# Kernel optimization log

Hardware: AMD Instinct MI355X
Metric: run time of the kernel (lower is better)

The kernel has to match this reference:

```python
import jax, jax.numpy as jnp
import numpy as np

B, S, D, F, E, K = 64, 512, 512, 2048, 8, 2


def setup_inputs() -> dict:
    key = jax.random.key(0)
    k0, k1, k2, k3 = jax.random.split(key, 4)
    x = jax.random.normal(k0, (B, S, D), dtype=jnp.float32)
    Wr = jax.random.normal(k1, (D, E), dtype=jnp.float32) * (D ** -0.5)
    br = jnp.zeros((E,), dtype=jnp.float32)
    W1 = jax.random.normal(k2, (E, D, F), dtype=jnp.float32) * (D ** -0.5)
    b1 = jnp.zeros((E, F), dtype=jnp.float32)
    W2 = jax.random.normal(k3, (E, F, D), dtype=jnp.float32) * (F ** -0.5)
    b2 = jnp.zeros((E, D), dtype=jnp.float32)
    return {"x": x, "Wr": Wr, "br": br, "W1": W1, "b1": b1, "W2": W2, "b2": b2}


def reference(x, Wr, br, W1, b1, W2, b2):
    orig_shape = x.shape
    t = x.reshape(-1, orig_shape[-1])          # [T, D] flattened tokens
    logits = t @ Wr + br                       # [T, E] router logits
    gates = jax.nn.softmax(logits, axis=-1)
    top_vals, top_idx = jax.lax.top_k(gates, K)      # [T, K]
    top_vals = top_vals / top_vals.sum(axis=-1, keepdims=True)
    # combine weight per (token, expert); zero unless expert is in token's top-k
    onehot = jax.nn.one_hot(top_idx, E, dtype=t.dtype)      # [T, K, E]
    combine = jnp.einsum('tk,tke->te', top_vals, onehot)    # [T, E]
    out = jnp.zeros_like(t)
    for e in range(E):  # small fixed expert count
        h = jax.nn.relu(t @ W1[e] + b1[e])     # [T, F]
        y = h @ W2[e] + b2[e]                  # [T, D]
        out = out + combine[:, e:e + 1] * y
    return out.reshape(orig_shape)
```

## Files before the change

kernel.cpp:

```cpp
#include <hip/hip_runtime.h>

#define T_TOKENS 32768
#define DIM 512
#define FDIM 2048
#define NEXP 8

typedef __attribute__((ext_vector_type(4))) float f32x4;
typedef __attribute__((ext_vector_type(8))) short bf16x8;

__device__ __forceinline__ unsigned short f2bf(float f) {
  unsigned int u = __float_as_uint(f);
  u += 0x7FFFu + ((u >> 16) & 1u);
  return (unsigned short)(u >> 16);
}

#define LGKM_BARRIER()                                        \
  do {                                                        \
    asm volatile("s_waitcnt lgkmcnt(0)" ::: "memory");        \
    __builtin_amdgcn_s_barrier();                             \
  } while (0)

__global__ void pack_w1_kernel(const float* __restrict__ W1, unsigned short* __restrict__ W1p) {
  __shared__ float L[512][17];
  const int b = blockIdx.x;
  const int e = b >> 7, ft = b & 127;
  const int t = threadIdx.x;
  const int c = t & 15, r0 = t >> 4;
  const float* src = W1 + (long)e * 512 * 2048 + ft * 16 + c;
  #pragma unroll
  for (int ch = 0; ch < 32; ch++) {
    int r = ch * 16 + r0;
    L[r][c] = src[(long)r * 2048];
  }
  __syncthreads();
  #pragma unroll
  for (int s = 0; s < 4; s++) {
    int slot = s * 256 + t;
    int kci = slot >> 6, l = slot & 63;
    unsigned short tmp[8];
    #pragma unroll
    for (int j = 0; j < 8; j++)
      tmp[j] = f2bf(L[kci * 32 + (l >> 4) * 8 + j][l & 15]);
    *(ushort4*)(W1p + ((long)b * 16 + kci) * 512 + l * 8)     = *(ushort4*)&tmp[0];
    *(ushort4*)(W1p + ((long)b * 16 + kci) * 512 + l * 8 + 4) = *(ushort4*)&tmp[4];
  }
}

__global__ void pack_w2_kernel(const float* __restrict__ W2, unsigned short* __restrict__ W2p) {
  __shared__ float L[512][17];
  const int b = blockIdx.x;
  const int e = b >> 5, dt = b & 31;
  const int t = threadIdx.x;
  const int c = t & 15, r0 = t >> 4;
  for (int ch = 0; ch < 4; ch++) {
    if (ch) __syncthreads();
    const float* src = W2 + ((long)e * 2048 + ch * 512) * 512 + dt * 16 + c;
    #pragma unroll
    for (int cc = 0; cc < 32; cc++) {
      int r = cc * 16 + r0;
      L[r][c] = src[(long)r * 512];
    }
    __syncthreads();
    #pragma unroll
    for (int s = 0; s < 4; s++) {
      int slot = s * 256 + t;
      int kciL = slot >> 6, l = slot & 63;
      unsigned short tmp[8];
      #pragma unroll
      for (int j = 0; j < 8; j++)
        tmp[j] = f2bf(L[kciL * 32 + (l >> 4) * 8 + j][l & 15]);
      long tt = (long)(e * 64 + ch * 16 + kciL) * 32 + dt;
      *(ushort4*)(W2p + tt * 512 + l * 8)     = *(ushort4*)&tmp[0];
      *(ushort4*)(W2p + tt * 512 + l * 8 + 4) = *(ushort4*)&tmp[4];
    }
  }
}

__global__ void router_kernel(const float* __restrict__ x, const float* __restrict__ Wr,
                              const float* __restrict__ br, int* __restrict__ counts,
                              int* __restrict__ tok_list, float* __restrict__ wt_list,
                              int* __restrict__ slots) {
  __shared__ float WrS[NEXP][DIM];
  __shared__ int lcnt[NEXP];
  __shared__ int lbase[NEXP];
  const int tid = threadIdx.x;
  for (int i = tid; i < NEXP * DIM; i += 256) {
    int e = i >> 9, d = i & (DIM - 1);
    WrS[e][d] = Wr[d * NEXP + e];
  }
  if (tid < NEXP) lcnt[tid] = 0;
  __syncthreads();

  const int t = blockIdx.x * 256 + tid;
  const float* xr = x + (long)t * DIM;
  float acc[NEXP];
  #pragma unroll
  for (int e = 0; e < NEXP; e++) acc[e] = br[e];
  for (int d = 0; d < DIM; d += 4) {
    const float4 xv = *(const float4*)(xr + d);
    #pragma unroll
    for (int e = 0; e < NEXP; e++)
      acc[e] += xv.x * WrS[e][d] + xv.y * WrS[e][d + 1] +
                xv.z * WrS[e][d + 2] + xv.w * WrS[e][d + 3];
  }
  int e0 = 0; float v0 = acc[0];
  #pragma unroll
  for (int e = 1; e < NEXP; e++) if (acc[e] > v0) { v0 = acc[e]; e0 = e; }
  int e1 = -1; float v1 = -3.4e38f;
  #pragma unroll
  for (int e = 0; e < NEXP; e++) if (e != e0 && acc[e] > v1) { v1 = acc[e]; e1 = e; }
  float w0 = 1.f / (1.f + __expf(v1 - v0));
  float w1 = 1.f - w0;

  int l0 = atomicAdd(&lcnt[e0], 1);
  int l1 = atomicAdd(&lcnt[e1], 1);
  __syncthreads();
  if (tid < NEXP) lbase[tid] = atomicAdd(&counts[tid], lcnt[tid]);
  __syncthreads();
  int s0 = lbase[e0] + l0;
  tok_list[e0 * T_TOKENS + s0] = t; wt_list[e0 * T_TOKENS + s0] = w0;
  int s1 = lbase[e1] + l1;
  tok_list[e1 * T_TOKENS + s1] = t; wt_list[e1 * T_TOKENS + s1] = w1;
  if (slots) {
    slots[2 * t]     = e0 * T_TOKENS + s0;
    slots[2 * t + 1] = e1 * T_TOKENS + s1;
  }
}

#define LD8(dst, ptr, kbase)                                    \
  _Pragma("unroll")                                             \
  for (int i = 0; i < 8; i++)                                   \
    dst[i] = *(const bf16x8*)((ptr) + (kbase + i) * 512);

#define MF8(src, kbase)                                                            \
  _Pragma("unroll")                                                                \
  for (int i = 0; i < 8; i++) {                                                    \
    int kci = (kbase) + i;                                                         \
    int xo = ((kci * 4 + g) ^ xsw) << 3;                                           \
    _Pragma("unroll")                                                              \
    for (int mt = 0; mt < 4; mt++) {                                               \
      bf16x8 af = *(const bf16x8*)&Xs[(mt * 16 + ln) * 512 + xo];                  \
      H[mt] = __builtin_amdgcn_mfma_f32_16x16x32_bf16(af, src[i], H[mt], 0, 0, 0); \
    }                                                                              \
  }

#define LD_W2(klbase)                                                             \
  _Pragma("unroll")                                                               \
  for (int kl = klbase; kl < klbase + 2; kl++) {                                  \
    const unsigned short* w2b =                                                   \
        W2p + ((long)((e * 64 + (fc >> 5) + kl) * 32 + wave * 4) * 64 + lane) * 8;\
    _Pragma("unroll")                                                             \
    for (int nt = 0; nt < 4; nt++)                                                \
      w2r[kl][nt] = *(const bf16x8*)(w2b + nt * 512);                             \
  }

template <bool USE_PARTIAL>
__global__ __launch_bounds__(512, 2) void ffn_kernel(
    const float* __restrict__ x,
    const unsigned short* __restrict__ W1p,
    const unsigned short* __restrict__ W2p,
    const float* __restrict__ b1, const float* __restrict__ b2,
    const int* __restrict__ counts,
    const int* __restrict__ tok_list, const float* __restrict__ wt_list,
    float* __restrict__ partial,
    float* __restrict__ out) {
  __shared__ unsigned short Xs[64 * 512];
  __shared__ unsigned short Hs[64 * 128];

  const int e = blockIdx.x & 7;
  const int tile = blockIdx.x >> 3;
  const int cnt = counts[e];
  const int m0 = tile * 64;
  if (m0 >= cnt) return;
  const int rows = min(64, cnt - m0);

  int pbase = 0;
  if (USE_PARTIAL) {
    #pragma unroll
    for (int i = 0; i < NEXP; i++) pbase += (i < e) ? counts[i] : 0;
  }

  const int tid = threadIdx.x;
  const int wave = tid >> 6, lane = tid & 63;
  const int g = lane >> 4, ln = lane & 15;

  #pragma unroll 4
  for (int c = tid; c < 64 * 128; c += 512) {
    int r = c >> 7, q = c & 127;
    ushort4 bv = {0, 0, 0, 0};
    if (r < rows) {
      int tk = tok_list[e * T_TOKENS + m0 + r];
      const f32x4 v = __builtin_nontemporal_load((const f32x4*)(x + (long)tk * DIM + q * 4));
      bv.x = f2bf(v[0]); bv.y = f2bf(v[1]); bv.z = f2bf(v[2]); bv.w = f2bf(v[3]);
    }
    int addr = r * 512 + ((((q >> 1) ^ (r & 7)) << 3) | ((q & 1) << 2));
    *(ushort4*)&Xs[addr] = bv;
  }
  LGKM_BARRIER();

  const f32x4 zero4 = {0.f, 0.f, 0.f, 0.f};
  f32x4 Yacc[4][4];
  #pragma unroll
  for (int a = 0; a < 4; a++)
    #pragma unroll
    for (int b = 0; b < 4; b++) Yacc[a][b] = zero4;

  const int xsw = ln & 7;

  const unsigned short* const w1b_first =
      W1p + ((long)(e * 128 + wave) * 16) * 512 + lane * 8;
  const unsigned short* w1b = w1b_first;

  bf16x8 wA[8], wB[8], w2r[4][4];
  LD8(wA, w1b, 0);

  for (int fc = 0; fc < FDIM; fc += 128) {
    unsigned short* Hp = &Hs[0];
    f32x4 H[4];
    #pragma unroll
    for (int mt = 0; mt < 4; mt++) H[mt] = zero4;

    LD8(wB, w1b, 8);
    __builtin_amdgcn_s_setprio(1);
    MF8(wA, 0);
    __builtin_amdgcn_s_setprio(0);
    LD_W2(0);
    __builtin_amdgcn_s_setprio(1);
    MF8(wB, 8);
    __builtin_amdgcn_s_setprio(0);
    w1b = (fc + 128 < FDIM) ? (w1b + 8 * 16 * 512) : w1b_first;
    LD8(wA, w1b, 0);

    LGKM_BARRIER();

    {
      float b1v = b1[e * FDIM + fc + wave * 16 + ln];
      int fl = wave * 16 + ln;
      #pragma unroll
      for (int mt = 0; mt < 4; mt++) {
        #pragma unroll
        for (int i = 0; i < 4; i++) {
          int m = mt * 16 + g * 4 + i;
          int addr = m * 128 + ((((fl >> 3) ^ (m & 7)) << 3) | (fl & 7));
          Hp[addr] = f2bf(fmaxf(H[mt][i] + b1v, 0.f));
        }
      }
    }
    LGKM_BARRIER();

    LD_W2(2);

    __builtin_amdgcn_s_setprio(1);
    #pragma unroll
    for (int kl = 0; kl < 4; kl++) {
      bf16x8 ha[4];
      #pragma unroll
      for (int mt = 0; mt < 4; mt++) {
        int m = mt * 16 + ln;
        ha[mt] = *(const bf16x8*)&Hp[m * 128 + ((((kl * 4 + g) ^ (m & 7)) << 3))];
      }
      #pragma unroll
      for (int nt = 0; nt < 4; nt++)
        #pragma unroll
        for (int mt = 0; mt < 4; mt++)
          Yacc[mt][nt] = __builtin_amdgcn_mfma_f32_16x16x32_bf16(ha[mt], w2r[kl][nt], Yacc[mt][nt], 0, 0, 0);
    }
    __builtin_amdgcn_s_setprio(0);
  }

  #pragma unroll
  for (int mt = 0; mt < 4; mt++) {
    #pragma unroll
    for (int i = 0; i < 4; i++) {
      int m = mt * 16 + g * 4 + i;
      if (m < rows) {
        float w = wt_list[e * T_TOKENS + m0 + m];
        if (USE_PARTIAL) {
          float* dst = partial + ((long)(pbase + m0 + m)) * DIM;
          #pragma unroll
          for (int nt = 0; nt < 4; nt++) {
            int d = (wave * 4 + nt) * 16 + ln;
            __builtin_nontemporal_store((Yacc[mt][nt][i] + b2[e * DIM + d]) * w, dst + d);
          }
        } else {
          int tk = tok_list[e * T_TOKENS + m0 + m];
          #pragma unroll
          for (int nt = 0; nt < 4; nt++) {
            int d = (wave * 4 + nt) * 16 + ln;
            float v = (Yacc[mt][nt][i] + b2[e * DIM + d]) * w;
            atomicAdd(out + (long)tk * DIM + d, v);
          }
        }
      }
    }
  }
}

__global__ __launch_bounds__(256) void combine_kernel(
    const float* __restrict__ partial, const int* __restrict__ slots,
    const int* __restrict__ counts, float* __restrict__ out) {
  __shared__ int pre[NEXP];
  if (threadIdx.x == 0) {
    int a = 0;
    #pragma unroll
    for (int i = 0; i < NEXP; i++) { pre[i] = a; a += counts[i]; }
  }
  __syncthreads();
  const int tid = threadIdx.x;
  const int tk = blockIdx.x * 2 + (tid >> 7);
  const int q = (tid & 127) << 2;
  const int2 sp = *(const int2*)(slots + 2 * tk);
  const long r0 = pre[sp.x >> 15] + (sp.x & (T_TOKENS - 1));
  const long r1 = pre[sp.y >> 15] + (sp.y & (T_TOKENS - 1));
  const f32x4 a = __builtin_nontemporal_load((const f32x4*)(partial + r0 * DIM + q));
  const f32x4 b = __builtin_nontemporal_load((const f32x4*)(partial + r1 * DIM + q));
  f32x4 r = a + b;
  __builtin_nontemporal_store(r, (f32x4*)(out + (long)tk * DIM + q));
}

extern "C" void kernel_launch(void* const* d_in, const int* in_sizes, int n_in,
                              void* d_out, int out_size, void* d_ws, size_t ws_size,
                              hipStream_t stream) {
  (void)in_sizes; (void)n_in; (void)out_size;
  const float* x  = (const float*)d_in[0];
  const float* Wr = (const float*)d_in[1];
  const float* br = (const float*)d_in[2];
  const float* W1 = (const float*)d_in[3];
  const float* b1 = (const float*)d_in[4];
  const float* W2 = (const float*)d_in[5];
  const float* b2 = (const float*)d_in[6];
  float* out = (float*)d_out;

  char* ws = (char*)d_ws;
  int*            counts   = (int*)(ws);
  int*            tok_list = (int*)(ws + 1024);
  float*          wt_list  = (float*)(ws + 1049600);
  int*            slots    = (int*)(ws + 2098176);
  unsigned short* W1p      = (unsigned short*)(ws + 2360320);
  unsigned short* W2p      = (unsigned short*)(ws + 19137536);
  float*          partial  = (float*)(ws + 35914752);
  const size_t need_partial = 35914752ull + (size_t)T_TOKENS * 2 * DIM * sizeof(float);
  const bool use_partial = ws_size >= need_partial;

  hipMemsetAsync(counts, 0, 1024, stream);
  pack_w1_kernel<<<NEXP * 128, 256, 0, stream>>>(W1, W1p);
  pack_w2_kernel<<<NEXP * 32, 256, 0, stream>>>(W2, W2p);

  if (use_partial) {
    router_kernel<<<T_TOKENS / 256, 256, 0, stream>>>(x, Wr, br, counts, tok_list, wt_list, slots);
    ffn_kernel<true><<<T_TOKENS / 64 * NEXP, 512, 0, stream>>>(
        x, W1p, W2p, b1, b2, counts, tok_list, wt_list, partial, out);
    combine_kernel<<<T_TOKENS / 2, 256, 0, stream>>>(partial, slots, counts, out);
  } else {
    hipMemsetAsync(out, 0, (size_t)T_TOKENS * DIM * sizeof(float), stream);
    router_kernel<<<T_TOKENS / 256, 256, 0, stream>>>(x, Wr, br, counts, tok_list, wt_list, nullptr);
    ffn_kernel<false><<<T_TOKENS / 64 * NEXP, 512, 0, stream>>>(
        x, W1p, W2p, b1, b2, counts, tok_list, wt_list, nullptr, out);
  }
}
```

Baseline: 633.3 us.

## Double F-chunk to 256 per iteration with two H tiles per wave

Each F-chunk iteration now covers 256 hidden columns instead of 128. Each wave computes two 16-column H tiles that share the same X fragment read from LDS. The change halves the number of barrier-separated iterations and the X LDS reads per MFMA. W2 fragments are streamed through two rotating register buffers inside the second GEMM, and the first W1 load is issued before the X staging. In exchange it doubles the Hs LDS buffer, raises register pressure, and makes the W2 loads per kl step less latency-hidden.

```diff
diff --git a/kernel.cpp b/kernel.cpp
--- a/kernel.cpp
+++ b/kernel.cpp
@@ -127,32 +127,34 @@
   }
 }
 
-#define LD8(dst, ptr, kbase)                                    \
-  _Pragma("unroll")                                             \
-  for (int i = 0; i < 8; i++)                                   \
-    dst[i] = *(const bf16x8*)((ptr) + (kbase + i) * 512);
-
-#define MF8(src, kbase)                                                            \
-  _Pragma("unroll")                                                                \
-  for (int i = 0; i < 8; i++) {                                                    \
-    int kci = (kbase) + i;                                                         \
-    int xo = ((kci * 4 + g) ^ xsw) << 3;                                           \
-    _Pragma("unroll")                                                              \
-    for (int mt = 0; mt < 4; mt++) {                                               \
-      bf16x8 af = *(const bf16x8*)&Xs[(mt * 16 + ln) * 512 + xo];                  \
-      H[mt] = __builtin_amdgcn_mfma_f32_16x16x32_bf16(af, src[i], H[mt], 0, 0, 0); \
-    }                                                                              \
-  }
-
-#define LD_W2(klbase)                                                             \
-  _Pragma("unroll")                                                               \
-  for (int kl = klbase; kl < klbase + 2; kl++) {                                  \
+#define LD4x2(dst, kbase)                                         \
+  _Pragma("unroll")                                               \
+  for (int i = 0; i < 4; i++) {                                   \
+    dst[i]     = *(const bf16x8*)(w1b + (kbase + i) * 512);       \
+    dst[4 + i] = *(const bf16x8*)(w1b + (16 + kbase + i) * 512);  \
+  }
+
+#define MF4x2(src, kbase)                                                            \
+  _Pragma("unroll")                                                                  \
+  for (int i = 0; i < 4; i++) {                                                      \
+    int kci = (kbase) + i;                                                           \
+    int xo = ((kci * 4 + g) ^ xsw) << 3;                                             \
+    _Pragma("unroll")                                                                \
+    for (int mt = 0; mt < 4; mt++) {                                                 \
+      bf16x8 af = *(const bf16x8*)&Xs[(mt * 16 + ln) * 512 + xo];                    \
+      HA[mt] = __builtin_amdgcn_mfma_f32_16x16x32_bf16(af, src[i],     HA[mt], 0, 0, 0); \
+      HB[mt] = __builtin_amdgcn_mfma_f32_16x16x32_bf16(af, src[4 + i], HB[mt], 0, 0, 0); \
+    }                                                                                \
+  }
+
+#define LD_W2B(buf, kl)                                                           \
+  do {                                                                            \
     const unsigned short* w2b =                                                   \
-        W2p + ((long)((e * 64 + (fc >> 5) + kl) * 32 + wave * 4) * 64 + lane) * 8;\
+        W2p + ((long)((e * 64 + (fc >> 5) + (kl)) * 32 + wave * 4) * 64 + lane) * 8;\
     _Pragma("unroll")                                                             \
     for (int nt = 0; nt < 4; nt++)                                                \
-      w2r[kl][nt] = *(const bf16x8*)(w2b + nt * 512);                             \
-  }
+      buf[nt] = *(const bf16x8*)(w2b + nt * 512);                                 \
+  } while (0)
 
 template <bool USE_PARTIAL>
 __global__ __launch_bounds__(512, 2) void ffn_kernel(
@@ -165,7 +167,7 @@
     float* __restrict__ partial,
     float* __restrict__ out) {
   __shared__ unsigned short Xs[64 * 512];
-  __shared__ unsigned short Hs[64 * 128];
+  __shared__ unsigned short Hs[64 * 256];
 
   const int e = blockIdx.x & 7;
   const int tile = blockIdx.x >> 3;
@@ -183,6 +185,13 @@
   const int tid = threadIdx.x;
   const int wave = tid >> 6, lane = tid & 63;
   const int g = lane >> 4, ln = lane & 15;
+
+  const unsigned short* const w1b_first =
+      W1p + ((long)(e * 128 + wave * 2) * 16) * 512 + lane * 8;
+  const unsigned short* w1b = w1b_first;
+
+  bf16x8 wP[8], wQ[8], w2rA[4], w2rB[4];
+  LD4x2(wP, 0);
 
   #pragma unroll 4
   for (int c = tid; c < 64 * 128; c += 512) {
@@ -207,63 +216,72 @@
 
   const int xsw = ln & 7;
 
-  const unsigned short* const w1b_first =
-      W1p + ((long)(e * 128 + wave) * 16) * 512 + lane * 8;
-  const unsigned short* w1b = w1b_first;
-
-  bf16x8 wA[8], wB[8], w2r[4][4];
-  LD8(wA, w1b, 0);
-
-  for (int fc = 0; fc < FDIM; fc += 128) {
-    unsigned short* Hp = &Hs[0];
-    f32x4 H[4];
-    #pragma unroll
-    for (int mt = 0; mt < 4; mt++) H[mt] = zero4;
-
-    LD8(wB, w1b, 8);
-    __builtin_amdgcn_s_setprio(1);
-    MF8(wA, 0);
-    __builtin_amdgcn_s_setprio(0);
-    LD_W2(0);
-    __builtin_amdgcn_s_setprio(1);
-    MF8(wB, 8);
-    __builtin_amdgcn_s_setprio(0);
-    w1b = (fc + 128 < FDIM) ? (w1b + 8 * 16 * 512) : w1b_first;
-    LD8(wA, w1b, 0);
+  for (int fc = 0; fc < FDIM; fc += 256) {
+    f32x4 HA[4], HB[4];
+    #pragma unroll
+    for (int mt = 0; mt < 4; mt++) { HA[mt] = zero4; HB[mt] = zero4; }
+
+    LD4x2(wQ, 4);
+    __builtin_amdgcn_s_setprio(1);
+    MF4x2(wP, 0);
+    __builtin_amdgcn_s_setprio(0);
+    LD4x2(wP, 8);
+    __builtin_amdgcn_s_setprio(1);
+    MF4x2(wQ, 4);
+    __builtin_amdgcn_s_setprio(0);
+    LD4x2(wQ, 12);
+    __builtin_amdgcn_s_setprio(1);
+    MF4x2(wP, 8);
+    __builtin_amdgcn_s_setprio(0);
+    LD_W2B(w2rA, 0);
+    __builtin_amdgcn_s_setprio(1);
+    MF4x2(wQ, 12);
+    __builtin_amdgcn_s_setprio(0);
+    LD_W2B(w2rB, 1);
+    w1b = (fc + 256 < FDIM) ? (w1b + 16 * 16 * 512) : w1b_first;
+    LD4x2(wP, 0);
 
     LGKM_BARRIER();
 
     {
-      float b1v = b1[e * FDIM + fc + wave * 16 + ln];
-      int fl = wave * 16 + ln;
+      float b1vA = b1[e * FDIM + fc + (wave * 2) * 16 + ln];
+      float b1vB = b1[e * FDIM + fc + (wave * 2 + 1) * 16 + ln];
+      int flA = (wave * 2) * 16 + ln;
+      int flB = flA + 16;
       #pragma unroll
       for (int mt = 0; mt < 4; mt++) {
         #pragma unroll
         for (int i = 0; i < 4; i++) {
           int m = mt * 16 + g * 4 + i;
-          int addr = m * 128 + ((((fl >> 3) ^ (m & 7)) << 3) | (fl & 7));
-          Hp[addr] = f2bf(fmaxf(H[mt][i] + b1v, 0.f));
+          int aA = m * 256 + ((((flA >> 3) ^ (m & 15)) << 3) | (flA & 7));
+          int aB = m * 256 + ((((flB >> 3) ^ (m & 15)) << 3) | (flB & 7));
+          Hs[aA] = f2bf(fmaxf(HA[mt][i] + b1vA, 0.f));
+          Hs[aB] = f2bf(fmaxf(HB[mt][i] + b1vB, 0.f));
         }
       }
     }
     LGKM_BARRIER();
 
-    LD_W2(2);
-
-    __builtin_amdgcn_s_setprio(1);
-    #pragma unroll
-    for (int kl = 0; kl < 4; kl++) {
+    __builtin_amdgcn_s_setprio(1);
+    #pragma unroll
+    for (int kl = 0; kl < 8; kl++) {
+      const bf16x8* w2c = (kl & 1) ? w2rB : w2rA;
       bf16x8 ha[4];
       #pragma unroll
       for (int mt = 0; mt < 4; mt++) {
         int m = mt * 16 + ln;
-        ha[mt] = *(const bf16x8*)&Hp[m * 128 + ((((kl * 4 + g) ^ (m & 7)) << 3))];
+        ha[mt] = *(const bf16x8*)&Hs[m * 256 + (((kl * 4 + g) ^ (m & 15)) << 3)];
       }
       #pragma unroll
       for (int nt = 0; nt < 4; nt++)
         #pragma unroll
         for (int mt = 0; mt < 4; mt++)
-          Yacc[mt][nt] = __builtin_amdgcn_mfma_f32_16x16x32_bf16(ha[mt], w2r[kl][nt], Yacc[mt][nt], 0, 0, 0);
+          Yacc[mt][nt] = __builtin_amdgcn_mfma_f32_16x16x32_bf16(ha[mt], w2c[nt], Yacc[mt][nt], 0, 0, 0);
+      if (kl < 6) {
+        __builtin_amdgcn_s_setprio(0);
+        if (kl & 1) { LD_W2B(w2rB, kl + 2); } else { LD_W2B(w2rA, kl + 2); }
+        __builtin_amdgcn_s_setprio(1);
+      }
     }
     __builtin_amdgcn_s_setprio(0);
   }
```

Measured after the change: 609.8 us. 1.04x faster.
